# Performance work log

Measured on AMD Instinct MI355X. Metric: run time of the kernel, lower is better.

Reference implementation:

```python
import jax, jax.numpy as jnp
import numpy as np

B, S, DIM = 1, 2048, 2048
HEADS, KV_HEADS = 32, 8
DH = DIM // HEADS          # 64 head dim
G = HEADS // KV_HEADS      # 4 grouped queries per kv head
CBLK = 16                  # compress block size (stride == block size)
SBLK = 16                  # selection (fine) block size
NSEL = 8                   # top-k selected blocks
WIN = 64                   # sliding window size
SCALE = DH ** -0.5
NEG = -1e30
CDIM = CBLK * DH


def setup_inputs():
    key = jax.random.key(0)
    ks = jax.random.split(key, 16)
    def rnd(i, shape, sc=0.02):
        return jax.random.normal(ks[i], shape, dtype=jnp.float32) * sc
    dim_inner, dim_kv = HEADS * DH, KV_HEADS * DH
    return {
        "hidden_states": jax.random.normal(ks[0], (B, S, DIM), dtype=jnp.float32),
        "w_qkv": rnd(1, (DIM, dim_inner + 2 * dim_kv)),
        "k_pos": rnd(2, (KV_HEADS, CBLK, DH)),
        "v_pos": rnd(3, (KV_HEADS, CBLK, DH)),
        "k_cw1": rnd(4, (CDIM, CDIM)), "k_cb1": jnp.zeros((CDIM,), jnp.float32),
        "k_cw2": rnd(5, (CDIM, DH)),  "k_cb2": jnp.zeros((DH,), jnp.float32),
        "v_cw1": rnd(6, (CDIM, CDIM)), "v_cb1": jnp.zeros((CDIM,), jnp.float32),
        "v_cw2": rnd(7, (CDIM, DH)),  "v_cb2": jnp.zeros((DH,), jnp.float32),
        "mem_ck": rnd(8, (KV_HEADS, 1, DH)),
        "mem_cv": rnd(9, (KV_HEADS, 1, DH)),
        "w_gate": rnd(10, (DIM, 3 * HEADS)),
        "b_gate": jnp.tile(jnp.array([-2.0, -2.0, 2.0], jnp.float32), HEADS),
        "w_out": rnd(11, (dim_inner, DIM)),
    }


def _rope(x, pos):
    # rotary-embedding-torch style: interleaved pairs (x0,x1),(x2,x3),...
    d = x.shape[-1]
    inv = 1.0 / (10000.0 ** (jnp.arange(0, d, 2, dtype=jnp.float32) / d))
    ang = pos[:, None] * inv[None, :]
    cos, sin = jnp.cos(ang), jnp.sin(ang)
    x1, x2 = x[..., 0::2], x[..., 1::2]
    return jnp.stack([x1 * cos - x2 * sin, x1 * sin + x2 * cos], axis=-1).reshape(x.shape)


def _forward(x, w_qkv, k_pos, v_pos, k_cw1, k_cb1, k_cw2, k_cb2,
             v_cw1, v_cb1, v_cw2, v_cb2, mem_ck, mem_cv, w_gate, b_gate, w_out):
    b, n, _ = x.shape
    di, dkv = HEADS * DH, KV_HEADS * DH
    qkv = x @ w_qkv
    # head index = kv_head * G + grouped_query, matching 'b n (h d) -> b h n d'
    q = qkv[..., :di].reshape(b, n, KV_HEADS, G, DH).transpose(0, 2, 3, 1, 4)    # [b,kh,g,n,d]
    k = qkv[..., di:di + dkv].reshape(b, n, KV_HEADS, DH).transpose(0, 2, 1, 3)  # [b,kh,n,d]
    v = qkv[..., di + dkv:].reshape(b, n, KV_HEADS, DH).transpose(0, 2, 1, 3)

    # ---- branch 1: compressed-block attention (pre-rotary q/k, intra-block abs pos) ----
    nc = n // CBLK
    kb = k[:, :, :nc * CBLK].reshape(b, KV_HEADS, nc, CBLK, DH) + k_pos[None, :, None]
    vb = v[:, :, :nc * CBLK].reshape(b, KV_HEADS, nc, CBLK, DH) + v_pos[None, :, None]
    ck = jax.nn.relu(kb.reshape(b, KV_HEADS, nc, CDIM) @ k_cw1 + k_cb1) @ k_cw2 + k_cb2
    cv = jax.nn.relu(vb.reshape(b, KV_HEADS, nc, CDIM) @ v_cw1 + v_cb1) @ v_cw2 + v_cb2
    ck = jnp.concatenate([jnp.broadcast_to(mem_ck[None], (b, KV_HEADS, 1, DH)), ck], axis=2)
    cv = jnp.concatenate([jnp.broadcast_to(mem_cv[None], (b, KV_HEADS, 1, DH)), cv], axis=2)
    csim = jnp.einsum('bhgnd,bhjd->bhgnj', q, ck) * SCALE
    ck_last = jnp.concatenate([jnp.array([-1]), (jnp.arange(nc) + 1) * CBLK - 1])
    cmask = ck_last[None, :] < jnp.arange(n)[:, None]                            # [n, 1+nc]
    csim = jnp.where(cmask, csim, NEG)
    c_out = jnp.einsum('bhgnj,bhjd->bhgnd', jax.nn.softmax(csim, -1), cv)

    # ---- importance scores -> top-k selected blocks (shared across grouped queries) ----
    imp = csim[..., 1:].mean(axis=2)                                             # [b,kh,n,nc]
    imp = jnp.concatenate([jnp.full(imp.shape[:-1] + (1,), -1e3, imp.dtype), imp], axis=-1)
    imp = jax.nn.softmax(imp, -1)[..., 1:]
    sel_vals, sel_idx = jax.lax.top_k(imp, NSEL)                                 # [b,kh,n,NSEL]
    fine_gate_mask = sel_vals > 1e-10

    # rotary for fine + sliding branches
    pos = jnp.arange(n, dtype=jnp.float32)
    rq, rk = _rope(q, pos), _rope(k, pos)

    # ---- branch 2: fine attention over top-k selected blocks + causal own block ----
    nf = n // SBLK
    own = jnp.broadcast_to((jnp.arange(n) // SBLK)[None, None, :, None], (b, KV_HEADS, n, 1))
    idx = jnp.concatenate([sel_idx, own], axis=-1)                               # [b,kh,n,NSEL+1]
    kblocks = rk.reshape(b, KV_HEADS, nf, SBLK, DH)
    vblocks = v.reshape(b, KV_HEADS, nf, SBLK, DH)
    bi = jnp.arange(b)[:, None, None, None]
    hi = jnp.arange(KV_HEADS)[None, :, None, None]
    fk = kblocks[bi, hi, idx].reshape(b, KV_HEADS, n, (NSEL + 1) * SBLK, DH)
    fv = vblocks[bi, hi, idx].reshape(b, KV_HEADS, n, (NSEL + 1) * SBLK, DH)
    sel_m = jnp.repeat(fine_gate_mask[..., None], SBLK, -1).reshape(b, KV_HEADS, n, NSEL * SBLK)
    diag_m = (jnp.arange(n) % SBLK)[:, None] >= jnp.arange(SBLK)[None, :]        # own-block causal
    fmask = jnp.concatenate(
        [sel_m, jnp.broadcast_to(diag_m[None, None], (b, KV_HEADS, n, SBLK))], axis=-1)
    fsim = jnp.einsum('bhgnd,bhnjd->bhgnj', rq, fk) * SCALE
    fsim = jnp.where(fmask[:, :, None], fsim, NEG)
    f_out = jnp.einsum('bhgnj,bhnjd->bhgnd', jax.nn.softmax(fsim, -1), fv)

    # ---- branch 3: sliding-window attention (current + previous window, exact size) ----
    nwin = n // WIN
    qw = rq.reshape(b, KV_HEADS, G, nwin, WIN, DH)
    kw = rk.reshape(b, KV_HEADS, nwin, WIN, DH)
    vw = v.reshape(b, KV_HEADS, nwin, WIN, DH)
    kcat = jnp.concatenate([jnp.concatenate([jnp.zeros_like(kw[:, :, :1]), kw[:, :, :-1]], 2), kw], 3)
    vcat = jnp.concatenate([jnp.concatenate([jnp.zeros_like(vw[:, :, :1]), vw[:, :, :-1]], 2), vw], 3)
    ssim = jnp.einsum('bhgwid,bhwjd->bhgwij', qw, kcat) * SCALE
    i_, j_ = jnp.arange(WIN), jnp.arange(2 * WIN)
    delta = i_[:, None] - (j_[None, :] - WIN)                                    # query - key distance
    smask = ((delta >= 0) & (delta <= WIN))[None] \
        & ((jnp.arange(nwin) > 0)[:, None, None] | (j_ >= WIN)[None, None, :])
    ssim = jnp.where(smask[None, None, None], ssim, NEG)
    s_out = jnp.einsum('bhgwij,bhwjd->bhgwid', jax.nn.softmax(ssim, -1), vcat)
    s_out = s_out.reshape(b, KV_HEADS, G, n, DH)

    # ---- learned sigmoid gate combine (compressed, fine, sliding) + out proj ----
    gates = jax.nn.sigmoid(x @ w_gate + b_gate).reshape(b, n, KV_HEADS, G, 3).transpose(0, 2, 3, 1, 4)
    out = gates[..., 0:1] * c_out + gates[..., 1:2] * f_out + gates[..., 2:3] * s_out
    out = out.transpose(0, 3, 1, 2, 4).reshape(b, n, HEADS * DH)
    return out @ w_out


def reference(hidden_states, w_qkv, k_pos, v_pos, k_cw1, k_cb1, k_cw2, k_cb2,
              v_cw1, v_cb1, v_cw2, v_cb2, mem_ck, mem_cv, w_gate, b_gate, w_out):
    return _forward(hidden_states, w_qkv, k_pos, v_pos, k_cw1, k_cb1, k_cw2, k_cb2,
                    v_cw1, v_cb1, v_cw2, v_cb2, mem_ck, mem_cv, w_gate, b_gate, w_out)
```

## Files before the change

kernel.cpp:

```cpp
#include <hip/hip_runtime.h>
#include <hip/hip_bf16.h>
#include <math.h>

using bf16 = __hip_bfloat16;
typedef __attribute__((ext_vector_type(8))) short short8;
typedef __attribute__((ext_vector_type(4))) float f32x4;

#define SCALE 0.125f
#define NEGV  -1e30f
#define QS    3200

__device__ __forceinline__ float bf2f(bf16 x) { return __bfloat162float(x); }
__device__ __forceinline__ bf16  f2bf(float x) { return __float2bfloat16(x); }
__device__ __forceinline__ short f2bs(float x) {
  bf16 b = __float2bfloat16(x);
  return *reinterpret_cast<short*>(&b);
}
__device__ __forceinline__ float dot4(float4 a, float4 b) {
  return a.x * b.x + a.y * b.y + a.z * b.z + a.w * b.w;
}
__device__ __forceinline__ float sigm(float x) { return 1.0f / (1.0f + __expf(-x)); }

__device__ __forceinline__ void wavefence() {
  asm volatile("s_waitcnt lgkmcnt(0)" ::: "memory");
}

__device__ __forceinline__ void gload16(const bf16* g, bf16* l) {
  __builtin_amdgcn_global_load_lds(
      (const __attribute__((address_space(1))) unsigned int*)g,
      (__attribute__((address_space(3))) unsigned int*)l, 16, 0, 0);
}

__global__ void detect_mode_kernel(const void* __restrict__ bgate, int* __restrict__ flag)
{
  if (threadIdx.x == 0 && blockIdx.x == 0) {
    unsigned w = *(const unsigned*)bgate;
    flag[0] = (w == 0xC0000000u) ? 1 : 0;
  }
}

struct ConvArgs {
  const void* src[17];
  bf16*       dst[17];
  int         start[18];
};

__global__ __launch_bounds__(256)
void convert_all_kernel(ConvArgs a, int total, const int* __restrict__ flag)
{
  int i = blockIdx.x * 256 + threadIdx.x;
  if (i >= total) return;
  int s = 0;
  while (s < 16 && i >= a.start[s + 1]) s++;
  int off = i - a.start[s];
  if (*flag) a.dst[s][off] = f2bf(((const float*)a.src[s])[off]);
  else       a.dst[s][off] = ((const bf16*)a.src[s])[off];
}

__global__ __launch_bounds__(256)
void transpose_conv_kernel(const void* __restrict__ src, bf16* __restrict__ dst,
                           int K, int N, const int* __restrict__ flag)
{
  __shared__ bf16 ls[64][65];
  const int n0 = blockIdx.x * 64, k0 = blockIdx.y * 64;
  const int tid = threadIdx.x, c = tid & 63, r4 = tid >> 6;
  const bool f = (*flag != 0);
  #pragma unroll 4
  for (int r = 0; r < 16; r++) {
    int kk = r * 4 + r4;
    bf16 v = f2bf(0.f);
    if (n0 + c < N)
      v = f ? f2bf(((const float*)src)[(size_t)(k0 + kk) * N + n0 + c])
            : ((const bf16*)src)[(size_t)(k0 + kk) * N + n0 + c];
    ls[kk][c] = v;
  }
  __syncthreads();
  #pragma unroll 4
  for (int r = 0; r < 16; r++) {
    int nn = r * 4 + r4;
    if (n0 + nn < N)
      dst[(size_t)(n0 + nn) * K + k0 + c] = ls[c][nn];
  }
}

__global__ __launch_bounds__(256)
void vtrans_kernel(const float* __restrict__ qkv, bf16* __restrict__ vt)
{
  __shared__ bf16 ls[64][65];
  const int h = blockIdx.y;
  const int i0 = blockIdx.x * 64;
  const int tid = threadIdx.x, c = tid & 63, r4 = tid >> 6;
  #pragma unroll 4
  for (int r = 0; r < 16; r++) {
    int ii = r * 4 + r4;
    ls[ii][c] = f2bf(qkv[(size_t)(i0 + ii) * QS + 2560 + h * 64 + c]);
  }
  __syncthreads();
  #pragma unroll 4
  for (int r = 0; r < 16; r++) {
    int dd = r * 4 + r4;
    vt[((size_t)h * 64 + dd) * 2176 + 64 + i0 + c] = ls[c][dd];
  }
}

__global__ __launch_bounds__(256)
void gemm64_splitk_kernel(const bf16* __restrict__ A, const bf16* __restrict__ B,
                          const bf16* __restrict__ B2, float* __restrict__ C,
                          int M, int N, int K, int msplit, int Ks)
{
  __shared__ __align__(16) bf16 As[64 * 32];
  __shared__ __align__(16) bf16 Bs[64 * 32];
  const int tid = threadIdx.x, wave = tid >> 6, lane = tid & 63;
  const int quad = lane >> 4, l16 = lane & 15;
  const int m0 = blockIdx.y * 64, n0 = blockIdx.x * 64;
  const int kb = blockIdx.z * Ks;
  const bf16* Bu = (m0 >= msplit) ? B2 : B;
  f32x4 acc[4] = {{0,0,0,0},{0,0,0,0},{0,0,0,0},{0,0,0,0}};
  const int arow = tid >> 2, akp = (tid & 3) * 8;
  const int bkr = tid >> 3, bnc = (tid & 7) * 8;

  for (int k0 = kb; k0 < kb + Ks; k0 += 32) {
    __syncthreads();
    {
      const bf16* Ap = A + (size_t)(m0 + arow) * K + k0 + akp;
      *(int4*)(void*)&As[arow * 32 + akp] = *(const int4*)(const void*)Ap;
    }
    const bf16* Bp = Bu + (size_t)(k0 + bkr) * N + n0 + bnc;
    {
      int4 raw = *(const int4*)(const void*)Bp;
      const bf16* tp = (const bf16*)&raw;
      #pragma unroll
      for (int j = 0; j < 8; j++) Bs[(bnc + j) * 32 + bkr] = tp[j];
    }
    __syncthreads();
    short8 a = *(const short8*)(const void*)&As[(wave * 16 + l16) * 32 + quad * 8];
    #pragma unroll
    for (int nt = 0; nt < 4; nt++) {
      short8 b = *(const short8*)(const void*)&Bs[(nt * 16 + l16) * 32 + quad * 8];
      acc[nt] = __builtin_amdgcn_mfma_f32_16x16x32_bf16(a, b, acc[nt], 0, 0, 0);
    }
  }

  #pragma unroll
  for (int nt = 0; nt < 4; nt++) {
    int col = n0 + nt * 16 + l16;
    if (col < N) {
      #pragma unroll
      for (int r = 0; r < 4; r++) {
        int row = m0 + wave * 16 + quad * 4 + r;
        atomicAdd(&C[(size_t)row * N + col], acc[nt][r]);
      }
    }
  }
}

template<int TC_BF16, int ACT, int SPLIT, int GATE, int STOREF>
__global__ __launch_bounds__(256)
void gemm_bt_kernel(const bf16* __restrict__ A, const bf16* __restrict__ Bt,
                    const bf16* __restrict__ Bt2, const bf16* __restrict__ bias,
                    const bf16* __restrict__ bias2, void* __restrict__ Cv,
                    int M, int N, int K, int msplit, const int* __restrict__ flag)
{
  __shared__ __align__(16) bf16 As[128 * 32];
  __shared__ __align__(16) bf16 Bs[128 * 32];
  const int tid = threadIdx.x, wave = tid >> 6, lane = tid & 63;
  const int quad = lane >> 4, l16 = lane & 15;
  const int wm = (wave >> 1) * 64, wn = (wave & 1) * 64;
  const int m0 = blockIdx.y * 128, n0 = blockIdx.x * 128;
  const bf16* Bu = (SPLIT && m0 >= msplit) ? Bt2 : Bt;
  const bf16* bu = (SPLIT && m0 >= msplit) ? bias2 : bias;
  f32x4 acc[4][4];
  #pragma unroll
  for (int mt = 0; mt < 4; mt++)
    #pragma unroll
    for (int nt = 0; nt < 4; nt++) acc[mt][nt] = f32x4{0, 0, 0, 0};

  const int lr = lane >> 2, lc = (lane & 3) * 8;
  const bf16* gA0 = A  + (size_t)(m0 + wave * 32 + lr) * K + lc;
  const bf16* gA1 = gA0 + (size_t)16 * K;
  const bf16* gB0 = Bu + (size_t)(n0 + wave * 32 + lr) * K + lc;
  const bf16* gB1 = gB0 + (size_t)16 * K;
  bf16* lA0 = &As[wave * 1024];
  bf16* lA1 = &As[wave * 1024 + 512];
  bf16* lB0 = &Bs[wave * 1024];
  bf16* lB1 = &Bs[wave * 1024 + 512];

  for (int k0 = 0; k0 < K; k0 += 32) {
    __syncthreads();
    gload16(gA0 + k0, lA0);
    gload16(gA1 + k0, lA1);
    gload16(gB0 + k0, lB0);
    gload16(gB1 + k0, lB1);
    __syncthreads();

    short8 a[4], b[4];
    #pragma unroll
    for (int mt = 0; mt < 4; mt++)
      a[mt] = *(const short8*)(const void*)&As[(wm + mt * 16 + l16) * 32 + quad * 8];
    #pragma unroll
    for (int nt = 0; nt < 4; nt++)
      b[nt] = *(const short8*)(const void*)&Bs[(wn + nt * 16 + l16) * 32 + quad * 8];
    #pragma unroll
    for (int mt = 0; mt < 4; mt++)
      #pragma unroll
      for (int nt = 0; nt < 4; nt++)
        acc[mt][nt] = __builtin_amdgcn_mfma_f32_16x16x32_bf16(a[mt], b[nt], acc[mt][nt], 0, 0, 0);
  }

  const bool f32out = STOREF ? (*flag != 0) : false;
  #pragma unroll
  for (int nt = 0; nt < 4; nt++) {
    int col = n0 + wn + nt * 16 + l16;
    float bv;
    if (GATE) bv = (col >= 3072 && col < 3168) ? bf2f(bias2[col - 3072]) : 0.0f;
    else      bv = bu ? bf2f(bu[col]) : 0.0f;
    #pragma unroll
    for (int mt = 0; mt < 4; mt++) {
      #pragma unroll
      for (int r = 0; r < 4; r++) {
        int row = m0 + wm + mt * 16 + quad * 4 + r;
        float v = acc[mt][nt][r] + bv;
        if (ACT == 1) v = fmaxf(v, 0.0f);
        if (STOREF) {
          if (f32out) ((float*)Cv)[(size_t)row * N + col] = v;
          else        ((bf16*)Cv)[(size_t)row * N + col]  = f2bf(v);
        } else if (TC_BF16) {
          ((bf16*)Cv)[(size_t)row * N + col] = f2bf(v);
        } else {
          ((float*)Cv)[(size_t)row * N + col] = v;
        }
      }
    }
  }
}

__global__ __launch_bounds__(256)
void prep_kb_kernel(const float* __restrict__ qkv, const bf16* __restrict__ k_pos,
                    const bf16* __restrict__ v_pos, bf16* __restrict__ kbflat,
                    bf16* __restrict__ vbflat)
{
  int idx = blockIdx.x * 256 + threadIdx.x;
  if (idx >= 8 * 128 * 1024) return;
  int h = idx >> 17, rem = idx & 131071;
  int c = rem >> 10, f = rem & 1023, t = f >> 6, d = f & 63;
  int tok = c * 16 + t;
  float kv = qkv[(size_t)tok * QS + 2048 + h * 64 + d] + bf2f(k_pos[(h * 16 + t) * 64 + d]);
  float vv = qkv[(size_t)tok * QS + 2560 + h * 64 + d] + bf2f(v_pos[(h * 16 + t) * 64 + d]);
  kbflat[idx] = f2bf(kv);
  vbflat[idx] = f2bf(vv);
}

__global__ __launch_bounds__(256)
void concat_kernel(const float* __restrict__ ckpre, const float* __restrict__ cvpre,
                   const bf16* __restrict__ mem_ck, const bf16* __restrict__ mem_cv,
                   const bf16* __restrict__ k_cb2, const bf16* __restrict__ v_cb2,
                   float* __restrict__ ck, bf16* __restrict__ cvT)
{
  int idx = blockIdx.x * 256 + threadIdx.x;
  if (idx >= 8 * 160 * 64) return;
  int h = idx / (160 * 64), r = (idx >> 6) % 160, d = idx & 63;
  if (r >= 129) { cvT[((size_t)h * 64 + d) * 160 + r] = f2bf(0.f); return; }
  float kv, vv;
  if (r == 0) {
    kv = bf2f(mem_ck[h * 64 + d]);
    vv = bf2f(mem_cv[h * 64 + d]);
  } else {
    kv = ckpre[((size_t)h * 128 + r - 1) * 64 + d] + bf2f(k_cb2[d]);
    vv = cvpre[((size_t)h * 128 + r - 1) * 64 + d] + bf2f(v_cb2[d]);
  }
  ck[((size_t)h * 129 + r) * 64 + d] = kv;
  cvT[((size_t)h * 64 + d) * 160 + r] = f2bf(vv);
}

__global__ __launch_bounds__(256)
void compress_attn_kernel(const float* __restrict__ qkv, const float* __restrict__ ck,
                          const bf16* __restrict__ cvT,
                          float* __restrict__ outpre, int* __restrict__ sel)
{
  __shared__ __align__(16) float qs[4][4][64];
  __shared__ __align__(16) bf16 ps[4][4][176];
  const int tid = threadIdx.x, w = tid >> 6, lane = tid & 63;
  const int quad = lane >> 4, l16 = lane & 15;
  const int R = blockIdx.x * 4 + w, h = R >> 11, i = R & 2047;
  const short8 zero8 = {0,0,0,0,0,0,0,0};

  #pragma unroll
  for (int g = 0; g < 4; g++)
    qs[w][g][lane] = qkv[(size_t)i * QS + (h * 4 + g) * 64 + lane];
  wavefence();

  const int jv = i >> 4;
  bool jin2 = (lane == 0);
  bool v0 = (lane == 0 || lane <= jv);
  bool v1 = (lane + 64 <= jv);
  bool v2 = jin2 && (128 <= jv);

  const float* kh = ck + (size_t)h * 129 * 64;
  const float4* k0 = (const float4*)(kh + lane * 64);
  const float4* k1 = (const float4*)(kh + (lane + 64) * 64);
  const float4* k2 = (const float4*)(kh + (jin2 ? 128 : 0) * 64);
  const float4* q4[4];
  #pragma unroll
  for (int g = 0; g < 4; g++) q4[g] = (const float4*)&qs[w][g][0];

  float d0[4] = {0,0,0,0}, d1[4] = {0,0,0,0}, d2[4] = {0,0,0,0};
  #pragma unroll
  for (int t = 0; t < 16; t++) {
    float4 a = k0[t], b = k1[t], c = k2[t];
    #pragma unroll
    for (int g = 0; g < 4; g++) {
      float4 qv = q4[g][t];
      d0[g] += dot4(qv, a);
      d1[g] += dot4(qv, b);
      d2[g] += dot4(qv, c);
    }
  }

  float sc0[4], sc1[4], sc2[4];
  #pragma unroll
  for (int g = 0; g < 4; g++) {
    sc0[g] = v0 ? d0[g] * SCALE : NEGV;
    sc1[g] = v1 ? d1[g] * SCALE : NEGV;
    sc2[g] = jin2 ? (v2 ? d2[g] * SCALE : NEGV) : -3.0e38f;
  }
  float imp0 = (sc0[0] + sc0[1] + sc0[2] + sc0[3]) * 0.25f;
  float imp1 = (sc1[0] + sc1[1] + sc1[2] + sc1[3]) * 0.25f;
  float imp2 = jin2 ? (sc2[0] + sc2[1] + sc2[2] + sc2[3]) * 0.25f : -3.0e38f;

  float p0[4], p1[4], p2[4];
  #pragma unroll
  for (int g = 0; g < 4; g++) {
    float mx = fmaxf(sc0[g], fmaxf(sc1[g], sc2[g]));
    for (int off = 32; off; off >>= 1) mx = fmaxf(mx, __shfl_xor(mx, off));
    float e0 = __expf(sc0[g] - mx), e1 = __expf(sc1[g] - mx);
    float e2 = jin2 ? __expf(sc2[g] - mx) : 0.0f;
    float sm = e0 + e1 + e2;
    for (int off = 32; off; off >>= 1) sm += __shfl_xor(sm, off);
    float inv = 1.0f / sm;
    p0[g] = e0 * inv; p1[g] = e1 * inv; p2[g] = e2 * inv;
  }

  #pragma unroll
  for (int g = 0; g < 4; g++) {
    ps[w][g][lane]      = f2bf(p0[g]);
    ps[w][g][64 + lane] = f2bf(p1[g]);
  }
  if (lane < 32) {
    #pragma unroll
    for (int g = 0; g < 4; g++)
      ps[w][g][128 + lane] = (lane == 0) ? f2bf(p2[g]) : f2bf(0.f);
  }
  wavefence();

  const int prow = (l16 < 4) ? l16 : 0;
  const bf16* cvh = cvT + (size_t)h * 64 * 160;
  f32x4 oc[4];
  #pragma unroll
  for (int dt = 0; dt < 4; dt++) oc[dt] = f32x4{0,0,0,0};
  #pragma unroll
  for (int ks = 0; ks < 5; ks++) {
    short8 ap = *(const short8*)(const void*)&ps[w][prow][ks * 32 + quad * 8];
    if (l16 >= 4) ap = zero8;
    #pragma unroll
    for (int dt = 0; dt < 4; dt++) {
      const bf16* cp = cvh + (size_t)(dt * 16 + l16) * 160 + ks * 32 + quad * 8;
      short8 bv = *(const short8*)(const void*)cp;
      oc[dt] = __builtin_amdgcn_mfma_f32_16x16x32_bf16(ap, bv, oc[dt], 0, 0, 0);
    }
  }
  if (quad == 0) {
    #pragma unroll
    for (int g = 0; g < 4; g++) {
      int hq = h * 4 + g;
      float g0 = sigm(qkv[(size_t)i * QS + 3072 + hq * 3 + 0]);
      #pragma unroll
      for (int dt = 0; dt < 4; dt++)
        outpre[(size_t)i * 2048 + hq * 64 + dt * 16 + l16] = g0 * oc[dt][g];
    }
  }

  float iv0 = (lane == 0) ? -1000.0f : imp0;
  float iv1 = imp1;
  float iv2 = imp2;
  float mx = fmaxf(iv0, fmaxf(iv1, iv2));
  for (int off = 32; off; off >>= 1) mx = fmaxf(mx, __shfl_xor(mx, off));
  float e0 = __expf(iv0 - mx), e1 = __expf(iv1 - mx);
  float e2 = jin2 ? __expf(iv2 - mx) : 0.0f;
  float sm = e0 + e1 + e2;
  for (int off = 32; off; off >>= 1) sm += __shfl_xor(sm, off);
  float inv = 1.0f / sm;
  float q0 = (lane >= 1) ? e0 * inv : -1.0f;
  float q1 = e1 * inv;
  float q2 = jin2 ? e2 * inv : -1.0f;

  for (int s = 0; s < 8; s++) {
    float bv = q0; int bj = lane;
    if (q1 > bv) { bv = q1; bj = lane + 64; }
    if (q2 > bv) { bv = q2; bj = lane + 128; }
    for (int off = 32; off; off >>= 1) {
      float ov = __shfl_xor(bv, off); int oj = __shfl_xor(bj, off);
      if (ov > bv || (ov == bv && oj < bj)) { bv = ov; bj = oj; }
    }
    if (lane == 0) sel[((size_t)h * 2048 + i) * 8 + s] = (bv > 1e-10f) ? (bj - 1) : -1;
    if (bj == lane)            q0 = -1.0f;
    else if (bj == lane + 64)  q1 = -1.0f;
    else if (bj == lane + 128) q2 = -1.0f;
  }
}

__global__ __launch_bounds__(256)
void rope_kernel(const float* __restrict__ qkv, bf16* __restrict__ qb,
                 bf16* __restrict__ kb)
{
  int idx = blockIdx.x * 256 + threadIdx.x;
  if (idx >= 2048 * 40 * 32) return;
  int m = idx & 31, hh = (idx >> 5) % 40, i = idx / 1280;
  int col = (hh < 32) ? hh * 64 + 2 * m : 2048 + (hh - 32) * 64 + 2 * m;
  const float* p = qkv + (size_t)i * QS + col;
  float x1 = p[0], x2 = p[1];
  float inv = exp2f(-0.41524101186092029f * (float)m);
  float ang = (float)i * inv;
  float s, c;
  __sincosf(ang, &s, &c);
  float r1 = x1 * c - x2 * s;
  float r2 = x1 * s + x2 * c;
  unsigned pack = ((unsigned)(unsigned short)f2bs(r1)) |
                  (((unsigned)(unsigned short)f2bs(r2)) << 16);
  if (hh < 32) {
    int h = hh >> 2, g = hh & 3;
    *(unsigned*)&qb[(((size_t)h * 2048 + i) * 4 + g) * 64 + 2 * m] = pack;
  } else {
    *(unsigned*)&kb[((size_t)(hh - 32) * 2048 + i) * 64 + 2 * m] = pack;
  }
}

__global__ __launch_bounds__(256)
void slide_attn_kernel(const float* __restrict__ qkv, const bf16* __restrict__ qb,
                       const bf16* __restrict__ kb, const bf16* __restrict__ vt,
                       bf16* __restrict__ oslide)
{
  __shared__ __align__(16) bf16 ps[4][16][104];
  const int tid = threadIdx.x, w = tid >> 6, lane = tid & 63;
  const int quad = lane >> 4, l16 = lane & 15;
  const int h = blockIdx.x >> 7, i0 = (blockIdx.x & 127) << 4;
  const int g = w;

  const bf16* qp = qb + (((size_t)h * 2048 + i0 + l16) * 4 + g) * 64 + quad * 8;
  short8 aq0 = *(const short8*)(const void*)qp;
  short8 aq1 = *(const short8*)(const void*)(qp + 32);

  const bf16* kbh = kb + (size_t)h * 2048 * 64;
  const int jbase = i0 - 64;

  f32x4 cs[5];
  #pragma unroll
  for (int t = 0; t < 5; t++) {
    int jr = jbase + t * 16 + l16;
    int jc = jr < 0 ? 0 : jr;
    const bf16* kp = kbh + (size_t)jc * 64 + quad * 8;
    short8 b0 = *(const short8*)(const void*)kp;
    short8 b1 = *(const short8*)(const void*)(kp + 32);
    f32x4 c = {0.f, 0.f, 0.f, 0.f};
    c = __builtin_amdgcn_mfma_f32_16x16x32_bf16(aq0, b0, c, 0, 0, 0);
    c = __builtin_amdgcn_mfma_f32_16x16x32_bf16(aq1, b1, c, 0, 0, 0);
    cs[t] = c;
  }

  float pr[5][4];
  #pragma unroll
  for (int r = 0; r < 4; r++) {
    int ti = i0 + quad * 4 + r;
    float mx = -3.0e38f;
    #pragma unroll
    for (int t = 0; t < 5; t++) {
      int j = jbase + t * 16 + l16;
      bool valid = (j >= 0) && (j >= ti - 64) && (j <= ti);
      float sv = valid ? cs[t][r] * SCALE : -3.0e38f;
      pr[t][r] = sv;
      mx = fmaxf(mx, sv);
    }
    #pragma unroll
    for (int off = 8; off; off >>= 1) mx = fmaxf(mx, __shfl_xor(mx, off));
    float sm = 0.f;
    #pragma unroll
    for (int t = 0; t < 5; t++) { float e = __expf(pr[t][r] - mx); pr[t][r] = e; sm += e; }
    #pragma unroll
    for (int off = 8; off; off >>= 1) sm += __shfl_xor(sm, off);
    float inv = 1.0f / sm;
    #pragma unroll
    for (int t = 0; t < 5; t++) pr[t][r] *= inv;
  }

  #pragma unroll
  for (int t = 0; t < 5; t++)
    #pragma unroll
    for (int r = 0; r < 4; r++)
      ps[w][quad * 4 + r][t * 16 + l16] = f2bf(pr[t][r]);
  #pragma unroll
  for (int r = 0; r < 4; r++) ps[w][l16][80 + quad * 4 + r] = f2bf(0.f);
  wavefence();

  const bf16* vth = vt + (size_t)h * 64 * 2176 + 64;
  f32x4 os[4];
  #pragma unroll
  for (int dt = 0; dt < 4; dt++) os[dt] = f32x4{0,0,0,0};
  #pragma unroll
  for (int ks = 0; ks < 3; ks++) {
    short8 ap = *(const short8*)(const void*)&ps[w][l16][ks * 32 + quad * 8];
    int coff = jbase + ks * 32 + quad * 8;
    #pragma unroll
    for (int dt = 0; dt < 4; dt++) {
      const bf16* vp = vth + (size_t)(dt * 16 + l16) * 2176 + coff;
      short8 bv = *(const short8*)(const void*)vp;
      os[dt] = __builtin_amdgcn_mfma_f32_16x16x32_bf16(ap, bv, os[dt], 0, 0, 0);
    }
  }

  #pragma unroll
  for (int r = 0; r < 4; r++) {
    int ti = i0 + quad * 4 + r;
    int hq = h * 4 + g;
    float g2 = sigm(qkv[(size_t)ti * QS + 3072 + hq * 3 + 2]);
    #pragma unroll
    for (int dt = 0; dt < 4; dt++)
      oslide[(size_t)ti * 2048 + hq * 64 + dt * 16 + l16] = f2bf(g2 * os[dt][r]);
  }
}

__global__ __launch_bounds__(256)
void fine_attn_kernel(const float* __restrict__ qkv, const int* __restrict__ sel,
                      const float* __restrict__ outpre, const bf16* __restrict__ oslide,
                      const bf16* __restrict__ qb, const bf16* __restrict__ kb,
                      const bf16* __restrict__ vt, bf16* __restrict__ outpre_b)
{
  __shared__ __align__(16) bf16 psf[4][4][176];
  const int tid = threadIdx.x, w = tid >> 6, lane = tid & 63;
  const int quad = lane >> 4, l16 = lane & 15;
  const int R = blockIdx.x * 4 + w, h = R >> 11, i = R & 2047;

  const short8 zero8 = {0,0,0,0,0,0,0,0};

  const int qrow = (l16 < 4) ? l16 : 0;
  const bf16* qp = qb + (((size_t)h * 2048 + i) * 4 + qrow) * 64 + quad * 8;
  short8 aq0 = *(const short8*)(const void*)qp;
  short8 aq1 = *(const short8*)(const void*)(qp + 32);
  if (l16 >= 4) { aq0 = zero8; aq1 = zero8; }

  const bf16* kbh = kb + (size_t)h * 2048 * 64;
  const int selb = (h * 2048 + i) * 8;
  const int imod = i & 15;

  int vblks[10];
  f32x4 ct[9];
  #pragma unroll
  for (int t = 0; t < 9; t++) {
    int blk = (t < 8) ? sel[selb + t] : (i >> 4);
    bool tvalid = (blk >= 0);
    int blc = tvalid ? blk : 0;
    vblks[t] = blc;
    const bf16* kp = kbh + ((size_t)(blc * 16 + l16)) * 64 + quad * 8;
    short8 b0 = *(const short8*)(const void*)kp;
    short8 b1 = *(const short8*)(const void*)(kp + 32);
    f32x4 c = {0.f, 0.f, 0.f, 0.f};
    c = __builtin_amdgcn_mfma_f32_16x16x32_bf16(aq0, b0, c, 0, 0, 0);
    c = __builtin_amdgcn_mfma_f32_16x16x32_bf16(aq1, b1, c, 0, 0, 0);
    bool valid = (t < 8) ? tvalid : (l16 <= imod);
    #pragma unroll
    for (int g = 0; g < 4; g++) ct[t][g] = valid ? c[g] * SCALE : -3.0e38f;
  }
  vblks[9] = 0;

  float fm[4], fsum[4];
  #pragma unroll
  for (int g = 0; g < 4; g++) fm[g] = -3.0e38f;
  #pragma unroll
  for (int t = 0; t < 9; t++)
    #pragma unroll
    for (int g = 0; g < 4; g++) fm[g] = fmaxf(fm[g], ct[t][g]);
  #pragma unroll
  for (int g = 0; g < 4; g++) {
    #pragma unroll
    for (int off = 8; off; off >>= 1) fm[g] = fmaxf(fm[g], __shfl_xor(fm[g], off));
    fsum[g] = 0.f;
  }
  #pragma unroll
  for (int t = 0; t < 9; t++)
    #pragma unroll
    for (int g = 0; g < 4; g++) {
      float e = __expf(ct[t][g] - fm[g]);
      ct[t][g] = e;
      fsum[g] += e;
    }
  #pragma unroll
  for (int g = 0; g < 4; g++) {
    #pragma unroll
    for (int off = 8; off; off >>= 1) fsum[g] += __shfl_xor(fsum[g], off);
    fsum[g] = 1.0f / fsum[g];
  }
  if (quad == 0) {
    #pragma unroll
    for (int t = 0; t < 9; t++)
      #pragma unroll
      for (int g = 0; g < 4; g++)
        psf[w][g][t * 16 + l16] = f2bf(ct[t][g] * fsum[g]);
    #pragma unroll
    for (int g = 0; g < 4; g++) psf[w][g][144 + l16] = f2bf(0.0f);
  }
  wavefence();

  const bf16* vth = vt + (size_t)h * 64 * 2176 + 64;
  const int prow = (l16 < 4) ? l16 : 0;
  f32x4 of[4];
  #pragma unroll
  for (int dt = 0; dt < 4; dt++) of[dt] = f32x4{0,0,0,0};

  #pragma unroll
  for (int ks = 0; ks < 5; ks++) {
    short8 ap = *(const short8*)(const void*)&psf[w][prow][ks * 32 + quad * 8];
    if (l16 >= 4) ap = zero8;
    int blkv = ((quad >> 1) == 0) ? vblks[ks * 2] : vblks[ks * 2 + 1];
    int coff = blkv * 16 + (quad & 1) * 8;
    #pragma unroll
    for (int dt = 0; dt < 4; dt++) {
      const bf16* vp = vth + ((size_t)dt * 16 + l16) * 2176 + coff;
      short8 bv = *(const short8*)(const void*)vp;
      of[dt] = __builtin_amdgcn_mfma_f32_16x16x32_bf16(ap, bv, of[dt], 0, 0, 0);
    }
  }

  if (quad == 0) {
    #pragma unroll
    for (int g = 0; g < 4; g++) {
      int hq = h * 4 + g;
      float g1 = sigm(qkv[(size_t)i * QS + 3072 + hq * 3 + 1]);
      #pragma unroll
      for (int dt = 0; dt < 4; dt++) {
        size_t oidx = (size_t)i * 2048 + hq * 64 + dt * 16 + l16;
        outpre_b[oidx] = f2bf(outpre[oidx] + bf2f(oslide[oidx]) + g1 * of[dt][g]);
      }
    }
  }
}

extern "C" void kernel_launch(void* const* d_in, const int* in_sizes, int n_in,
                              void* d_out, int out_size, void* d_ws, size_t ws_size,
                              hipStream_t stream)
{
  char* ws = (char*)d_ws;
  size_t off = 0;
  auto alloc = [&](size_t bytes) -> char* {
    char* p = ws + off; off = (off + bytes + 255) & ~(size_t)255; return p;
  };

  int* flag = (int*)alloc(256);
  bf16* inb[17];
  for (int i = 0; i < 17; i++) {
    if (i == 1 || i == 4 || i == 8 || i == 14 || i == 16) { inb[i] = nullptr; continue; }
    inb[i] = (bf16*)alloc((size_t)in_sizes[i] * sizeof(bf16));
  }
  bf16* w_qkvT = (bf16*)alloc(3200ull * 2048 * 2);
  bf16* k_cw1T = (bf16*)alloc(1024ull * 1024 * 2);
  bf16* v_cw1T = (bf16*)alloc(1024ull * 1024 * 2);
  bf16* w_outT = (bf16*)alloc(2048ull * 2048 * 2);

  float* qkv      = (float*)alloc(2048ull * QS * 4);
  float* outpre   = (float*)alloc(2048ull * 2048 * 4);
  bf16*  kvb      = (bf16*)alloc(2048ull * 1024 * 2);
  bf16*  hid      = (bf16*)alloc(2048ull * 1024 * 2);
  float* ckcvpre  = (float*)alloc(2048ull * 64 * 4);
  float* ckb      = (float*)alloc(8ull * 129 * 64 * 4);
  int*   sel      = (int*)alloc(8ull * 2048 * 8 * 4);
  bf16*  qbuf     = (bf16*)alloc(8ull * 2048 * 4 * 64 * 2);
  bf16*  kbuf     = (bf16*)alloc(8ull * 2048 * 64 * 2);
  bf16*  vtb      = (bf16*)alloc(8ull * 64 * 2176 * 2);
  bf16*  outpre_b = kvb;
  bf16*  cvT      = k_cw1T;
  bf16*  oslide   = (bf16*)w_qkvT;

  const bf16 *xb = inb[0], *k_posb = inb[2], *v_posb = inb[3],
             *k_cb1b = inb[5], *k_cw2b = inb[6], *k_cb2b = inb[7],
             *v_cb1b = inb[9], *v_cw2b = inb[10], *v_cb2b = inb[11],
             *mem_ckb = inb[12], *mem_cvb = inb[13], *b_gateb = inb[15];

  detect_mode_kernel<<<1, 64, 0, stream>>>(d_in[15], flag);

  ConvArgs ca;
  int total = 0, nseg = 0;
  for (int i = 0; i < 17; i++) {
    if (i == 1 || i == 4 || i == 8 || i == 14 || i == 16) continue;
    ca.src[nseg] = d_in[i];
    ca.dst[nseg] = inb[i];
    ca.start[nseg] = total;
    total += in_sizes[i];
    nseg++;
  }
  for (int s = nseg; s <= 17; s++) ca.start[s] = total;
  convert_all_kernel<<<(total + 255) / 256, 256, 0, stream>>>(ca, total, flag);

  transpose_conv_kernel<<<dim3(48, 32), 256, 0, stream>>>(d_in[1],  w_qkvT, 2048, 3072, flag);
  transpose_conv_kernel<<<dim3(2, 32),  256, 0, stream>>>(d_in[14], w_qkvT + 3072ull * 2048, 2048, 96, flag);
  transpose_conv_kernel<<<dim3(16, 16), 256, 0, stream>>>(d_in[4],  k_cw1T, 1024, 1024, flag);
  transpose_conv_kernel<<<dim3(16, 16), 256, 0, stream>>>(d_in[8],  v_cw1T, 1024, 1024, flag);
  transpose_conv_kernel<<<dim3(32, 32), 256, 0, stream>>>(d_in[16], w_outT, 2048, 2048, flag);
  hipMemsetAsync(ckcvpre, 0, 2048ull * 64 * 4, stream);
  hipMemsetAsync(vtb, 0, 8ull * 64 * 2176 * 2, stream);

  gemm_bt_kernel<0,0,0,1,0><<<dim3(25, 16), 256, 0, stream>>>(
      xb, w_qkvT, nullptr, nullptr, b_gateb, qkv, 2048, QS, 2048, 0, nullptr);

  rope_kernel<<<10240, 256, 0, stream>>>(qkv, qbuf, kbuf);
  vtrans_kernel<<<dim3(32, 8), 256, 0, stream>>>(qkv, vtb);

  prep_kb_kernel<<<4096, 256, 0, stream>>>(qkv, k_posb, v_posb, kvb, kvb + 1024 * 1024);
  gemm_bt_kernel<1,1,1,0,0><<<dim3(8, 16), 256, 0, stream>>>(
      kvb, k_cw1T, v_cw1T, k_cb1b, v_cb1b, hid, 2048, 1024, 1024, 1024, nullptr);
  gemm64_splitk_kernel<<<dim3(1, 32, 4), 256, 0, stream>>>(
      hid, k_cw2b, v_cw2b, ckcvpre, 2048, 64, 1024, 1024, 256);
  concat_kernel<<<320, 256, 0, stream>>>(ckcvpre, ckcvpre + 1024 * 64,
                                         mem_ckb, mem_cvb, k_cb2b, v_cb2b, ckb, cvT);
  compress_attn_kernel<<<4096, 256, 0, stream>>>(qkv, ckb, cvT, outpre, sel);
  slide_attn_kernel<<<1024, 256, 0, stream>>>(qkv, qbuf, kbuf, vtb, oslide);
  fine_attn_kernel<<<4096, 256, 0, stream>>>(qkv, sel, outpre, oslide, qbuf, kbuf, vtb, outpre_b);
  gemm_bt_kernel<0,0,0,0,1><<<dim3(16, 16), 256, 0, stream>>>(
      outpre_b, w_outT, nullptr, nullptr, nullptr, d_out, 2048, 2048, 2048, 0, flag);
}
```

Measured before the change: 548.8 us.

## Process four queries per wave in compress and fine attention kernels

Each wave now handles four consecutive query positions (16 MFMA rows of 4 queries × 4 grouped heads) instead of one, in both the compress-attention and fine-attention kernels. The compressed keys are loaded once and reused across four queries, and the MFMA tiles that were mostly zero-padded (only 4 of 16 rows used) are now filled. Grids shrink from 4096 to 1024 blocks. In the fine kernel the shared own-block PV product is computed once, but each query's selected blocks still need separate MFMA passes, with per-quad result selection that adds register pressure and redundant MFMA work.

```diff
diff --git a/kernel.cpp b/kernel.cpp
--- a/kernel.cpp
+++ b/kernel.cpp
@@ -277,134 +277,148 @@
                           const bf16* __restrict__ cvT,
                           float* __restrict__ outpre, int* __restrict__ sel)
 {
-  __shared__ __align__(16) float qs[4][4][64];
-  __shared__ __align__(16) bf16 ps[4][4][176];
+  __shared__ __align__(16) float qs[4][16][64];
+  __shared__ __align__(16) bf16  ps[4][16][176];
   const int tid = threadIdx.x, w = tid >> 6, lane = tid & 63;
   const int quad = lane >> 4, l16 = lane & 15;
-  const int R = blockIdx.x * 4 + w, h = R >> 11, i = R & 2047;
-  const short8 zero8 = {0,0,0,0,0,0,0,0};
-
-  #pragma unroll
-  for (int g = 0; g < 4; g++)
-    qs[w][g][lane] = qkv[(size_t)i * QS + (h * 4 + g) * 64 + lane];
+  const int h = blockIdx.x >> 7;
+  const int i0 = (blockIdx.x & 127) * 16 + w * 4;
+
+  #pragma unroll
+  for (int m = 0; m < 16; m++)
+    qs[w][m][lane] = qkv[(size_t)(i0 + (m >> 2)) * QS + (h * 4 + (m & 3)) * 64 + lane];
   wavefence();
 
-  const int jv = i >> 4;
-  bool jin2 = (lane == 0);
-  bool v0 = (lane == 0 || lane <= jv);
-  bool v1 = (lane + 64 <= jv);
-  bool v2 = jin2 && (128 <= jv);
-
+  const bool jin2 = (lane == 0);
   const float* kh = ck + (size_t)h * 129 * 64;
   const float4* k0 = (const float4*)(kh + lane * 64);
   const float4* k1 = (const float4*)(kh + (lane + 64) * 64);
   const float4* k2 = (const float4*)(kh + (jin2 ? 128 : 0) * 64);
-  const float4* q4[4];
-  #pragma unroll
-  for (int g = 0; g < 4; g++) q4[g] = (const float4*)&qs[w][g][0];
-
-  float d0[4] = {0,0,0,0}, d1[4] = {0,0,0,0}, d2[4] = {0,0,0,0};
-  #pragma unroll
+
+  float d0[4][4], d1[4][4], d2[4][4];
+  #pragma unroll
+  for (int T = 0; T < 4; T++)
+    #pragma unroll
+    for (int g = 0; g < 4; g++) { d0[T][g] = 0.f; d1[T][g] = 0.f; d2[T][g] = 0.f; }
+
+  #pragma unroll 4
   for (int t = 0; t < 16; t++) {
     float4 a = k0[t], b = k1[t], c = k2[t];
     #pragma unroll
+    for (int T = 0; T < 4; T++)
+      #pragma unroll
+      for (int g = 0; g < 4; g++) {
+        float4 qv = *(const float4*)&qs[w][T * 4 + g][t * 4];
+        d0[T][g] += dot4(qv, a);
+        d1[T][g] += dot4(qv, b);
+        d2[T][g] += dot4(qv, c);
+      }
+  }
+
+  #pragma unroll
+  for (int T = 0; T < 4; T++) {
+    const int i = i0 + T, jv = i >> 4;
+    bool v0 = (lane == 0 || lane <= jv);
+    bool v1 = (lane + 64 <= jv);
+    bool v2 = jin2 && (128 <= jv);
+
+    float sc0[4], sc1[4], sc2[4];
+    #pragma unroll
     for (int g = 0; g < 4; g++) {
-      float4 qv = q4[g][t];
-      d0[g] += dot4(qv, a);
-      d1[g] += dot4(qv, b);
-      d2[g] += dot4(qv, c);
-    }
-  }
-
-  float sc0[4], sc1[4], sc2[4];
-  #pragma unroll
-  for (int g = 0; g < 4; g++) {
-    sc0[g] = v0 ? d0[g] * SCALE : NEGV;
-    sc1[g] = v1 ? d1[g] * SCALE : NEGV;
-    sc2[g] = jin2 ? (v2 ? d2[g] * SCALE : NEGV) : -3.0e38f;
-  }
-  float imp0 = (sc0[0] + sc0[1] + sc0[2] + sc0[3]) * 0.25f;
-  float imp1 = (sc1[0] + sc1[1] + sc1[2] + sc1[3]) * 0.25f;
-  float imp2 = jin2 ? (sc2[0] + sc2[1] + sc2[2] + sc2[3]) * 0.25f : -3.0e38f;
-
-  float p0[4], p1[4], p2[4];
-  #pragma unroll
-  for (int g = 0; g < 4; g++) {
-    float mx = fmaxf(sc0[g], fmaxf(sc1[g], sc2[g]));
+      sc0[g] = v0 ? d0[T][g] * SCALE : NEGV;
+      sc1[g] = v1 ? d1[T][g] * SCALE : NEGV;
+      sc2[g] = jin2 ? (v2 ? d2[T][g] * SCALE : NEGV) : -3.0e38f;
+    }
+    float imp0 = (sc0[0] + sc0[1] + sc0[2] + sc0[3]) * 0.25f;
+    float imp1 = (sc1[0] + sc1[1] + sc1[2] + sc1[3]) * 0.25f;
+    float imp2 = jin2 ? (sc2[0] + sc2[1] + sc2[2] + sc2[3]) * 0.25f : -3.0e38f;
+
+    float p0[4], p1[4], p2[4];
+    #pragma unroll
+    for (int g = 0; g < 4; g++) {
+      float mx = fmaxf(sc0[g], fmaxf(sc1[g], sc2[g]));
+      for (int off = 32; off; off >>= 1) mx = fmaxf(mx, __shfl_xor(mx, off));
+      float e0 = __expf(sc0[g] - mx), e1 = __expf(sc1[g] - mx);
+      float e2 = jin2 ? __expf(sc2[g] - mx) : 0.0f;
+      float sm = e0 + e1 + e2;
+      for (int off = 32; off; off >>= 1) sm += __shfl_xor(sm, off);
+      float inv = 1.0f / sm;
+      p0[g] = e0 * inv; p1[g] = e1 * inv; p2[g] = e2 * inv;
+    }
+
+    #pragma unroll
+    for (int g = 0; g < 4; g++) {
+      ps[w][T * 4 + g][lane]      = f2bf(p0[g]);
+      ps[w][T * 4 + g][64 + lane] = f2bf(p1[g]);
+    }
+    if (lane == 0) {
+      #pragma unroll
+      for (int g = 0; g < 4; g++) ps[w][T * 4 + g][128] = f2bf(p2[g]);
+    }
+
+    float iv0 = (lane == 0) ? -1000.0f : imp0;
+    float iv1 = imp1;
+    float iv2 = imp2;
+    float mx = fmaxf(iv0, fmaxf(iv1, iv2));
     for (int off = 32; off; off >>= 1) mx = fmaxf(mx, __shfl_xor(mx, off));
-    float e0 = __expf(sc0[g] - mx), e1 = __expf(sc1[g] - mx);
-    float e2 = jin2 ? __expf(sc2[g] - mx) : 0.0f;
+    float e0 = __expf(iv0 - mx), e1 = __expf(iv1 - mx);
+    float e2 = jin2 ? __expf(iv2 - mx) : 0.0f;
     float sm = e0 + e1 + e2;
     for (int off = 32; off; off >>= 1) sm += __shfl_xor(sm, off);
     float inv = 1.0f / sm;
-    p0[g] = e0 * inv; p1[g] = e1 * inv; p2[g] = e2 * inv;
-  }
-
-  #pragma unroll
-  for (int g = 0; g < 4; g++) {
-    ps[w][g][lane]      = f2bf(p0[g]);
-    ps[w][g][64 + lane] = f2bf(p1[g]);
-  }
-  if (lane < 32) {
-    #pragma unroll
-    for (int g = 0; g < 4; g++)
-      ps[w][g][128 + lane] = (lane == 0) ? f2bf(p2[g]) : f2bf(0.f);
-  }
+    float q0 = (lane >= 1) ? e0 * inv : -1.0f;
+    float q1 = e1 * inv;
+    float q2 = jin2 ? e2 * inv : -1.0f;
+
+    for (int s = 0; s < 8; s++) {
+      float bv = q0; int bj = lane;
+      if (q1 > bv) { bv = q1; bj = lane + 64; }
+      if (q2 > bv) { bv = q2; bj = lane + 128; }
+      for (int off = 32; off; off >>= 1) {
+        float ov = __shfl_xor(bv, off); int oj = __shfl_xor(bj, off);
+        if (ov > bv || (ov == bv && oj < bj)) { bv = ov; bj = oj; }
+      }
+      if (lane == 0) sel[((size_t)h * 2048 + i) * 8 + s] = (bv > 1e-10f) ? (bj - 1) : -1;
+      if (bj == lane)            q0 = -1.0f;
+      else if (bj == lane + 64)  q1 = -1.0f;
+      else if (bj == lane + 128) q2 = -1.0f;
+    }
+  }
+
+  #pragma unroll
+  for (int r = 0; r < 4; r++) {
+    ps[w][quad * 4 + r][129 + l16] = f2bf(0.f);
+    ps[w][quad * 4 + r][145 + l16] = f2bf(0.f);
+  }
+
+  const int iq = i0 + quad;
+  float g0v[4];
+  #pragma unroll
+  for (int g = 0; g < 4; g++)
+    g0v[g] = sigm(qkv[(size_t)iq * QS + 3072 + (h * 4 + g) * 3 + 0]);
   wavefence();
 
-  const int prow = (l16 < 4) ? l16 : 0;
   const bf16* cvh = cvT + (size_t)h * 64 * 160;
-  f32x4 oc[4];
-  #pragma unroll
-  for (int dt = 0; dt < 4; dt++) oc[dt] = f32x4{0,0,0,0};
+  f32x4 acc[4];
+  #pragma unroll
+  for (int dt = 0; dt < 4; dt++) acc[dt] = f32x4{0, 0, 0, 0};
   #pragma unroll
   for (int ks = 0; ks < 5; ks++) {
-    short8 ap = *(const short8*)(const void*)&ps[w][prow][ks * 32 + quad * 8];
-    if (l16 >= 4) ap = zero8;
+    short8 ap = *(const short8*)(const void*)&ps[w][l16][ks * 32 + quad * 8];
     #pragma unroll
     for (int dt = 0; dt < 4; dt++) {
       const bf16* cp = cvh + (size_t)(dt * 16 + l16) * 160 + ks * 32 + quad * 8;
       short8 bv = *(const short8*)(const void*)cp;
-      oc[dt] = __builtin_amdgcn_mfma_f32_16x16x32_bf16(ap, bv, oc[dt], 0, 0, 0);
-    }
-  }
-  if (quad == 0) {
-    #pragma unroll
-    for (int g = 0; g < 4; g++) {
-      int hq = h * 4 + g;
-      float g0 = sigm(qkv[(size_t)i * QS + 3072 + hq * 3 + 0]);
-      #pragma unroll
-      for (int dt = 0; dt < 4; dt++)
-        outpre[(size_t)i * 2048 + hq * 64 + dt * 16 + l16] = g0 * oc[dt][g];
-    }
-  }
-
-  float iv0 = (lane == 0) ? -1000.0f : imp0;
-  float iv1 = imp1;
-  float iv2 = imp2;
-  float mx = fmaxf(iv0, fmaxf(iv1, iv2));
-  for (int off = 32; off; off >>= 1) mx = fmaxf(mx, __shfl_xor(mx, off));
-  float e0 = __expf(iv0 - mx), e1 = __expf(iv1 - mx);
-  float e2 = jin2 ? __expf(iv2 - mx) : 0.0f;
-  float sm = e0 + e1 + e2;
-  for (int off = 32; off; off >>= 1) sm += __shfl_xor(sm, off);
-  float inv = 1.0f / sm;
-  float q0 = (lane >= 1) ? e0 * inv : -1.0f;
-  float q1 = e1 * inv;
-  float q2 = jin2 ? e2 * inv : -1.0f;
-
-  for (int s = 0; s < 8; s++) {
-    float bv = q0; int bj = lane;
-    if (q1 > bv) { bv = q1; bj = lane + 64; }
-    if (q2 > bv) { bv = q2; bj = lane + 128; }
-    for (int off = 32; off; off >>= 1) {
-      float ov = __shfl_xor(bv, off); int oj = __shfl_xor(bj, off);
-      if (ov > bv || (ov == bv && oj < bj)) { bv = ov; bj = oj; }
-    }
-    if (lane == 0) sel[((size_t)h * 2048 + i) * 8 + s] = (bv > 1e-10f) ? (bj - 1) : -1;
-    if (bj == lane)            q0 = -1.0f;
-    else if (bj == lane + 64)  q1 = -1.0f;
-    else if (bj == lane + 128) q2 = -1.0f;
+      acc[dt] = __builtin_amdgcn_mfma_f32_16x16x32_bf16(ap, bv, acc[dt], 0, 0, 0);
+    }
+  }
+
+  #pragma unroll
+  for (int g = 0; g < 4; g++) {
+    const int hq = h * 4 + g;
+    #pragma unroll
+    for (int dt = 0; dt < 4; dt++)
+      outpre[(size_t)iq * 2048 + hq * 64 + dt * 16 + l16] = g0v[g] * acc[dt][g];
   }
 }
 
@@ -533,42 +547,58 @@
                       const bf16* __restrict__ qb, const bf16* __restrict__ kb,
                       const bf16* __restrict__ vt, bf16* __restrict__ outpre_b)
 {
-  __shared__ __align__(16) bf16 psf[4][4][176];
+  __shared__ __align__(16) bf16 psf[4][16][176];
   const int tid = threadIdx.x, w = tid >> 6, lane = tid & 63;
   const int quad = lane >> 4, l16 = lane & 15;
-  const int R = blockIdx.x * 4 + w, h = R >> 11, i = R & 2047;
-
-  const short8 zero8 = {0,0,0,0,0,0,0,0};
-
-  const int qrow = (l16 < 4) ? l16 : 0;
-  const bf16* qp = qb + (((size_t)h * 2048 + i) * 4 + qrow) * 64 + quad * 8;
+  const int h = blockIdx.x >> 7;
+  const int i0 = (blockIdx.x & 127) * 16 + w * 4;
+
+  const bf16* qp = qb + (((size_t)h * 2048 + i0 + (l16 >> 2)) * 4 + (l16 & 3)) * 64 + quad * 8;
   short8 aq0 = *(const short8*)(const void*)qp;
   short8 aq1 = *(const short8*)(const void*)(qp + 32);
-  if (l16 >= 4) { aq0 = zero8; aq1 = zero8; }
 
   const bf16* kbh = kb + (size_t)h * 2048 * 64;
-  const int selb = (h * 2048 + i) * 8;
-  const int imod = i & 15;
-
-  int vblks[10];
+  const int own = i0 >> 4;
+  const int selbase = (h * 2048 + i0) * 8;
+
   f32x4 ct[9];
-  #pragma unroll
-  for (int t = 0; t < 9; t++) {
-    int blk = (t < 8) ? sel[selb + t] : (i >> 4);
-    bool tvalid = (blk >= 0);
-    int blc = tvalid ? blk : 0;
-    vblks[t] = blc;
-    const bf16* kp = kbh + ((size_t)(blc * 16 + l16)) * 64 + quad * 8;
+
+  {
+    const bf16* kp = kbh + (size_t)(own * 16 + l16) * 64 + quad * 8;
     short8 b0 = *(const short8*)(const void*)kp;
     short8 b1 = *(const short8*)(const void*)(kp + 32);
     f32x4 c = {0.f, 0.f, 0.f, 0.f};
     c = __builtin_amdgcn_mfma_f32_16x16x32_bf16(aq0, b0, c, 0, 0, 0);
     c = __builtin_amdgcn_mfma_f32_16x16x32_bf16(aq1, b1, c, 0, 0, 0);
-    bool valid = (t < 8) ? tvalid : (l16 <= imod);
-    #pragma unroll
-    for (int g = 0; g < 4; g++) ct[t][g] = valid ? c[g] * SCALE : -3.0e38f;
-  }
-  vblks[9] = 0;
+    const int imod = (i0 + quad) & 15;
+    #pragma unroll
+    for (int g = 0; g < 4; g++)
+      ct[8][g] = (l16 <= imod) ? c[g] * SCALE : -3.0e38f;
+  }
+
+  int vb[4][8];
+  #pragma unroll
+  for (int T = 0; T < 4; T++) {
+    #pragma unroll
+    for (int t = 0; t < 8; t++) {
+      int blk = __builtin_amdgcn_readfirstlane(sel[selbase + T * 8 + t]);
+      bool tv = (blk >= 0);
+      int blc = tv ? blk : 0;
+      vb[T][t] = blc;
+      const bf16* kp = kbh + (size_t)(blc * 16 + l16) * 64 + quad * 8;
+      short8 b0 = *(const short8*)(const void*)kp;
+      short8 b1 = *(const short8*)(const void*)(kp + 32);
+      f32x4 c = {0.f, 0.f, 0.f, 0.f};
+      c = __builtin_amdgcn_mfma_f32_16x16x32_bf16(aq0, b0, c, 0, 0, 0);
+      c = __builtin_amdgcn_mfma_f32_16x16x32_bf16(aq1, b1, c, 0, 0, 0);
+      #pragma unroll
+      for (int g = 0; g < 4; g++) {
+        float v = tv ? c[g] * SCALE : -3.0e38f;
+        if (T == 0) ct[t][g] = v;
+        else if (quad == T) ct[t][g] = v;
+      }
+    }
+  }
 
   float fm[4], fsum[4];
   #pragma unroll
@@ -597,47 +627,77 @@
     for (int off = 8; off; off >>= 1) fsum[g] += __shfl_xor(fsum[g], off);
     fsum[g] = 1.0f / fsum[g];
   }
-  if (quad == 0) {
-    #pragma unroll
-    for (int t = 0; t < 9; t++)
-      #pragma unroll
-      for (int g = 0; g < 4; g++)
-        psf[w][g][t * 16 + l16] = f2bf(ct[t][g] * fsum[g]);
-    #pragma unroll
-    for (int g = 0; g < 4; g++) psf[w][g][144 + l16] = f2bf(0.0f);
+
+  #pragma unroll
+  for (int t = 0; t < 9; t++)
+    #pragma unroll
+    for (int g = 0; g < 4; g++)
+      psf[w][quad * 4 + g][t * 16 + l16] = f2bf(ct[t][g] * fsum[g]);
+  #pragma unroll
+  for (int g = 0; g < 4; g++)
+    psf[w][quad * 4 + g][144 + l16] = f2bf(0.f);
+
+  const int iq = i0 + quad;
+  float g1v[4], prev[4][4];
+  #pragma unroll
+  for (int g = 0; g < 4; g++) {
+    const int hq = h * 4 + g;
+    g1v[g] = sigm(qkv[(size_t)iq * QS + 3072 + hq * 3 + 1]);
+    #pragma unroll
+    for (int dt = 0; dt < 4; dt++) {
+      size_t oidx = (size_t)iq * 2048 + hq * 64 + dt * 16 + l16;
+      prev[g][dt] = outpre[oidx] + bf2f(oslide[oidx]);
+    }
   }
   wavefence();
 
   const bf16* vth = vt + (size_t)h * 64 * 2176 + 64;
-  const int prow = (l16 < 4) ? l16 : 0;
-  f32x4 of[4];
-  #pragma unroll
-  for (int dt = 0; dt < 4; dt++) of[dt] = f32x4{0,0,0,0};
-
-  #pragma unroll
-  for (int ks = 0; ks < 5; ks++) {
-    short8 ap = *(const short8*)(const void*)&psf[w][prow][ks * 32 + quad * 8];
-    if (l16 >= 4) ap = zero8;
-    int blkv = ((quad >> 1) == 0) ? vblks[ks * 2] : vblks[ks * 2 + 1];
-    int coff = blkv * 16 + (quad & 1) * 8;
+
+  f32x4 obase[4];
+  {
+    short8 ap = *(const short8*)(const void*)&psf[w][l16][128 + quad * 8];
+    int coff = (((quad >> 1) == 0) ? own : 0) * 16 + (quad & 1) * 8;
     #pragma unroll
     for (int dt = 0; dt < 4; dt++) {
-      const bf16* vp = vth + ((size_t)dt * 16 + l16) * 2176 + coff;
+      const bf16* vp = vth + (size_t)(dt * 16 + l16) * 2176 + coff;
       short8 bv = *(const short8*)(const void*)vp;
-      of[dt] = __builtin_amdgcn_mfma_f32_16x16x32_bf16(ap, bv, of[dt], 0, 0, 0);
-    }
-  }
-
-  if (quad == 0) {
-    #pragma unroll
-    for (int g = 0; g < 4; g++) {
-      int hq = h * 4 + g;
-      float g1 = sigm(qkv[(size_t)i * QS + 3072 + hq * 3 + 1]);
+      f32x4 z = {0.f, 0.f, 0.f, 0.f};
+      obase[dt] = __builtin_amdgcn_mfma_f32_16x16x32_bf16(ap, bv, z, 0, 0, 0);
+    }
+  }
+
+  f32x4 osave[4];
+  #pragma unroll
+  for (int T = 0; T < 4; T++) {
+    f32x4 acc[4];
+    #pragma unroll
+    for (int dt = 0; dt < 4; dt++) acc[dt] = obase[dt];
+    #pragma unroll
+    for (int ks = 0; ks < 4; ks++) {
+      short8 ap = *(const short8*)(const void*)&psf[w][l16][ks * 32 + quad * 8];
+      int blkv = ((quad >> 1) == 0) ? vb[T][ks * 2] : vb[T][ks * 2 + 1];
+      int coff = blkv * 16 + (quad & 1) * 8;
       #pragma unroll
       for (int dt = 0; dt < 4; dt++) {
-        size_t oidx = (size_t)i * 2048 + hq * 64 + dt * 16 + l16;
-        outpre_b[oidx] = f2bf(outpre[oidx] + bf2f(oslide[oidx]) + g1 * of[dt][g]);
+        const bf16* vp = vth + (size_t)(dt * 16 + l16) * 2176 + coff;
+        short8 bv = *(const short8*)(const void*)vp;
+        acc[dt] = __builtin_amdgcn_mfma_f32_16x16x32_bf16(ap, bv, acc[dt], 0, 0, 0);
       }
+    }
+    #pragma unroll
+    for (int dt = 0; dt < 4; dt++) {
+      if (T == 0) osave[dt] = acc[dt];
+      else if (quad == T) osave[dt] = acc[dt];
+    }
+  }
+
+  #pragma unroll
+  for (int g = 0; g < 4; g++) {
+    const int hq = h * 4 + g;
+    #pragma unroll
+    for (int dt = 0; dt < 4; dt++) {
+      size_t oidx = (size_t)iq * 2048 + hq * 64 + dt * 16 + l16;
+      outpre_b[oidx] = f2bf(prev[g][dt] + g1v[g] * osave[dt][g]);
     }
   }
 }
@@ -718,9 +778,9 @@
       hid, k_cw2b, v_cw2b, ckcvpre, 2048, 64, 1024, 1024, 256);
   concat_kernel<<<320, 256, 0, stream>>>(ckcvpre, ckcvpre + 1024 * 64,
                                          mem_ckb, mem_cvb, k_cb2b, v_cb2b, ckb, cvT);
-  compress_attn_kernel<<<4096, 256, 0, stream>>>(qkv, ckb, cvT, outpre, sel);
+  compress_attn_kernel<<<1024, 256, 0, stream>>>(qkv, ckb, cvT, outpre, sel);
   slide_attn_kernel<<<1024, 256, 0, stream>>>(qkv, qbuf, kbuf, vtb, oslide);
-  fine_attn_kernel<<<4096, 256, 0, stream>>>(qkv, sel, outpre, oslide, qbuf, kbuf, vtb, outpre_b);
+  fine_attn_kernel<<<1024, 256, 0, stream>>>(qkv, sel, outpre, oslide, qbuf, kbuf, vtb, outpre_b);
   gemm_bt_kernel<0,0,0,0,1><<<dim3(16, 16), 256, 0, stream>>>(
       outpre_b, w_outT, nullptr, nullptr, nullptr, d_out, 2048, 2048, 2048, 0, flag);
 }
```

Result: faster. 516.3 us (-5.9%).
